# Optimization experiments

Hardware: AMD Instinct MI355X
Metric: run time of the kernel (lower is better)

Reference implementation:

```python
import jax, jax.numpy as jnp
import numpy as np

TAU = 2.0
SG_ALPHA = 4.0  # spikingjelly surrogate.Sigmoid default alpha
BN_EPS = 1e-5


def _spike_fwd(x):
    s = (x >= 0.0).astype(x.dtype)
    return s, x


def _spike_bwd(x, g):
    sg = jax.nn.sigmoid(SG_ALPHA * x)
    return (g * SG_ALPHA * sg * (1.0 - sg),)


@jax.custom_vjp
def spike(x):
    return (x >= 0.0).astype(x.dtype)

spike.defvjp(_spike_fwd, _spike_bwd)


def lif(x_seq, v_th=1.0):
    """MultiStepLIFNode: v += (x - v)/tau (v_reset=0), hard reset, detach_reset.
    x_seq: [T, ...] -> spike train [T, ...]."""
    def step(v, x):
        v = v + (x - v) / TAU
        s = spike(v - v_th)
        v = v * (1.0 - jax.lax.stop_gradient(s))
        return v, s
    v0 = jnp.zeros_like(x_seq[0])
    _, s_seq = jax.lax.scan(step, v0, x_seq)
    return s_seq


def bn1d(x, p):
    """Eval-mode BatchNorm1d over channel dim. x: [M, C, N], p: [4, C] = gamma,beta,mean,var."""
    g, b, m, v = p[0], p[1], p[2], p[3]
    scale = g * jax.lax.rsqrt(v + BN_EPS)
    return (x - m[:, None]) * scale[:, None] + b[:, None]


def setup_inputs() -> dict:
    key = jax.random.key(0)
    ks = jax.random.split(key, 16)
    T, B, C, H, W = 4, 8, 256, 32, 32
    hid = 1024
    wscale = 1.0 / np.sqrt(C)
    inp = {
        "x": jax.random.normal(ks[0], (T, B, C, H, W), jnp.float32),
        "q_w": jax.random.normal(ks[1], (C, C), jnp.float32) * wscale,
        "q_bn": jax.random.uniform(ks[2], (4, C), jnp.float32, 0.1, 1.0),
        "k_w": jax.random.normal(ks[3], (C, C), jnp.float32) * wscale,
        "k_bn": jax.random.uniform(ks[4], (4, C), jnp.float32, 0.1, 1.0),
        "v_w": jax.random.normal(ks[5], (C, C), jnp.float32) * wscale,
        "v_bn": jax.random.uniform(ks[6], (4, C), jnp.float32, 0.1, 1.0),
        "proj_w": jax.random.normal(ks[7], (C, C), jnp.float32) * wscale,
        "proj_b": jax.random.normal(ks[8], (C,), jnp.float32) * 0.01,
        "proj_bn": jax.random.uniform(ks[9], (4, C), jnp.float32, 0.1, 1.0),
        "mlp1_w": jax.random.normal(ks[10], (hid, C), jnp.float32) * wscale,
        "mlp1_b": jax.random.normal(ks[11], (hid,), jnp.float32) * 0.01,
        "mlp1_bn": jax.random.uniform(ks[12], (4, hid), jnp.float32, 0.1, 1.0),
        "mlp2_w": jax.random.normal(ks[13], (C, hid), jnp.float32) * (1.0 / np.sqrt(hid)),
        "mlp2_b": jax.random.normal(ks[14], (C,), jnp.float32) * 0.01,
        "mlp2_bn": jax.random.uniform(ks[15], (4, C), jnp.float32, 0.1, 1.0),
    }
    return inp


def reference(x, q_w, q_bn, k_w, k_bn, v_w, v_bn, proj_w, proj_b, proj_bn,
              mlp1_w, mlp1_b, mlp1_bn, mlp2_w, mlp2_b, mlp2_bn):
    T, B, C, H, W = x.shape
    N = H * W
    heads = 8
    d = C // heads
    scale = 0.125

    # ---- SSA (FB_LiDiff_Attention) ----
    x2 = x.reshape(T * B, C, N)  # conv1x1 input

    def qkv_path(w, p):
        y = jnp.einsum('oc,mcn->mon', w, x2)           # conv1x1, no bias
        y = bn1d(y, p).reshape(T, B, C, N)
        s = lif(y)                                      # [T,B,C,N] spikes
        # -> [T,B,heads,N,d]
        return s.transpose(0, 1, 3, 2).reshape(T, B, N, heads, d).transpose(0, 1, 3, 2, 4)

    q = qkv_path(q_w, q_bn)
    k = qkv_path(k_w, k_bn)
    v = qkv_path(v_w, v_bn)

    kv = jnp.einsum('tbhnd,tbhne->tbhde', k, v)         # k^T @ v  [T,B,h,d,d]
    a = jnp.einsum('tbhnd,tbhde->tbhne', q, kv) * scale  # q @ kv  [T,B,h,N,d]
    a = a.transpose(0, 1, 2, 4, 3).reshape(T, B, C, N)   # transpose(3,4).reshape
    a = lif(a, v_th=0.5)

    p = jnp.einsum('oc,mcn->mon', proj_w, a.reshape(T * B, C, N)) + proj_b[:, None]
    p = bn1d(p, proj_bn).reshape(T, B, C, N)
    ssa = lif(p).reshape(T, B, C, W, H)  # note W,H swap as in source (H==W)

    x = x + ssa

    # ---- MLP (conv1x1 + BN + LIF, x2) ----
    h1 = jnp.einsum('oc,mcn->mon', mlp1_w, x.reshape(T * B, C, N)) + mlp1_b[:, None]
    hid = mlp1_w.shape[0]
    h1 = lif(bn1d(h1, mlp1_bn).reshape(T, B, hid, N))
    h2 = jnp.einsum('oc,mcn->mon', mlp2_w, h1.reshape(T * B, hid, N)) + mlp2_b[:, None]
    h2 = lif(bn1d(h2, mlp2_bn).reshape(T, B, C, N)).reshape(T, B, C, H, W)

    return x + h2
```

## Files before the change

kernel.cpp:

```cpp
#include <hip/hip_runtime.h>
#include <cstdint>
#include <cstddef>

#define TT 4
#define BB 8
#define CC 256
#define NN 1024
#define HEADS 8
#define DD 32
#define FIXCAP 262144u

typedef __attribute__((ext_vector_type(4))) float f32x4;
typedef __attribute__((ext_vector_type(8))) short s16x8;
typedef unsigned short u16;
typedef unsigned int   u32;

__device__ __forceinline__ u16 bf16_rne(float x) {
    u32 u = __float_as_uint(x);
    return (u16)((u + 0x7FFFu + ((u >> 16) & 1u)) >> 16);
}
__device__ __forceinline__ float bf16f(u16 h) {
    return __uint_as_float(((u32)h) << 16);
}

__global__ __launch_bounds__(64) void zero_counters(u32* c) {
    if (threadIdx.x < 4) c[threadIdx.x] = 0;
}


template<int OO, int CIN>
__global__ __launch_bounds__(256) void prep_split_fm(
    const float* __restrict__ src, u16* __restrict__ h, u16* __restrict__ l)
{
    const int id = blockIdx.x * 256 + threadIdx.x;
    if (id >= OO * CIN / 8) return;
    const int o = id / (CIN / 8), kq = id % (CIN / 8);
    const float* p = src + (size_t)o * CIN + kq * 8;
    s16x8 hh, ll;
#pragma unroll
    for (int e = 0; e < 8; ++e) {
        float f = p[e];
        u16 hb = bf16_rne(f);
        hh[e] = (short)hb;
        ll[e] = (short)bf16_rne(f - bf16f(hb));
    }
    const int lane = (kq & 3) * 16 + (o & 15);
    const size_t dst = (((size_t)(o >> 4) * (CIN / 32) + (kq >> 2)) * 64 + lane) * 8;
    *(s16x8*)&h[dst] = hh;
    *(s16x8*)&l[dst] = ll;
}

template<int K, int N>
__global__ __launch_bounds__(256) void trans_split_fm(
    const float* __restrict__ src, u16* __restrict__ dh, u16* __restrict__ dl)
{
    __shared__ float tile[64][65];
    const int tid = threadIdx.x;
    const int n0 = blockIdx.x * 64, k0 = blockIdx.y * 64, m = blockIdx.z;
    for (int i = tid; i < 4096; i += 256) {
        int kk = i >> 6, nn = i & 63;
        tile[kk][nn] = src[((size_t)m * K + k0 + kk) * N + n0 + nn];
    }
    __syncthreads();
    const size_t plane = (size_t)m * (N / 16) * (K / 32) * 512;
    for (int it = tid; it < 512; it += 256) {
        const int nn = it >> 3, kq = it & 7;
        s16x8 hh, ll;
#pragma unroll
        for (int e = 0; e < 8; ++e) {
            float f = tile[kq * 8 + e][nn];
            u16 hb = bf16_rne(f);
            hh[e] = (short)hb;
            ll[e] = (short)bf16_rne(f - bf16f(hb));
        }
        const int n = n0 + nn;
        const int ks = (k0 >> 5) + (kq >> 2), lk = kq & 3;
        const size_t dst = plane + (((size_t)(n >> 4) * (K / 32) + ks) * 64
                                    + lk * 16 + (n & 15)) * 8;
        *(s16x8*)&dh[dst] = hh;
        *(s16x8*)&dl[dst] = ll;
    }
}

template<int K, int N>
__global__ __launch_bounds__(256) void trans_u16_fm(
    const u16* __restrict__ src, u16* __restrict__ dst)
{
    __shared__ u16 tile[64][72];
    const int tid = threadIdx.x;
    const int n0 = blockIdx.x * 64, k0 = blockIdx.y * 64, m = blockIdx.z;
    for (int i = tid; i < 4096; i += 256) {
        int kk = i >> 6, nn = i & 63;
        tile[kk][nn] = src[((size_t)m * K + k0 + kk) * N + n0 + nn];
    }
    __syncthreads();
    const size_t plane = (size_t)m * (N / 16) * (K / 32) * 512;
    for (int it = tid; it < 512; it += 256) {
        const int nn = it >> 3, kq = it & 7;
        s16x8 hh;
#pragma unroll
        for (int e = 0; e < 8; ++e) hh[e] = (short)tile[kq * 8 + e][nn];
        const int n = n0 + nn;
        const int ks = (k0 >> 5) + (kq >> 2), lk = kq & 3;
        const size_t d = plane + (((size_t)(n >> 4) * (K / 32) + ks) * 64
                                  + lk * 16 + (n & 15)) * 8;
        *(s16x8*)&dst[d] = hh;
    }
}

__global__ __launch_bounds__(256) void prep_bn(
    const float* qbn, const float* kbn, const float* vbn, const float* pbn,
    const float* m1bn, const float* m2bn,
    const float* pb, const float* m1b, const float* m2b,
    float2* __restrict__ bnf, double* __restrict__ bnd)
{
    int c = blockIdx.x * 256 + threadIdx.x;
    if (c >= 2304) return;
    const float* bn; int ch, O; double bi = 0.0;
    if (c < 1024) {
        int s = c >> 8; ch = c & 255; O = 256;
        bn = s == 0 ? qbn : s == 1 ? kbn : s == 2 ? vbn : pbn;
        if (s == 3) bi = (double)pb[ch];
    } else if (c < 2048) { ch = c - 1024; O = 1024; bn = m1bn; bi = (double)m1b[ch]; }
    else                 { ch = c - 2048; O = 256;  bn = m2bn; bi = (double)m2b[ch]; }
    double g = (double)bn[0*O+ch], be = (double)bn[1*O+ch];
    double mu = (double)bn[2*O+ch], var = (double)bn[3*O+ch];
    double sd = g / sqrt(var + 1e-5);
    bnf[c] = make_float2((float)sd, (float)((bi - mu) * sd + be));
    bnd[c] = sd;
}

template<bool SPLIT_IN, int CIN, int OUT_MODE, bool TRIPLE, int O>
__global__ __launch_bounds__(256, 2) void conv_kernel(
    const u16* __restrict__ XTH, const u16* __restrict__ XTL,
    const u16* __restrict__ WH0, const u16* __restrict__ WL0,
    const u16* __restrict__ WH1, const u16* __restrict__ WL1,
    const u16* __restrict__ WH2, const u16* __restrict__ WL2,
    const float2* __restrict__ bnf,
    void* __restrict__ O0_, void* __restrict__ O1_, void* __restrict__ O2_,
    const float* __restrict__ base,
    u32* __restrict__ cnt, u32* __restrict__ list)
{
    constexpr float EPS = 3e-4f;
    constexpr u32 OT = TRIPLE ? 12 : O / 64;
    constexpr u32 NWG = OT * 16 * 8;
    constexpr int NS = CIN / 32;
    constexpr u32 KS = (u32)(CIN / 32);
    __shared__ float pre[2 * 64 * 64];

    const int tid  = threadIdx.x;
    const int lane = tid & 63;
    const int wave = tid >> 6;
    const int lr   = lane & 15;
    const int lk   = lane >> 4;

    const u32 orig = blockIdx.x + OT * (blockIdx.y + 16u * blockIdx.z);
    const u32 flat = (orig & 7u) * (NWG >> 3) + (orig >> 3);
    const u32 otile = flat % OT;
    const u32 rem   = flat / OT;
    const int n0 = (int)(rem & 15u) * 64;
    const int b  = (int)(rem >> 4);

    int o0, sel;
    const u16 *WH, *WL;
    void* Out_;
    if constexpr (TRIPLE) {
        sel = (int)(otile >> 2);
        o0 = (int)(otile & 3) * 64;
        WH = sel==0?WH0:sel==1?WH1:WH2;  WL = sel==0?WL0:sel==1?WL1:WL2;
        Out_ = sel==0?O0_:sel==1?O1_:O2_;
    } else {
        sel = 0; o0 = (int)otile * 64; WH = WH0; WL = WL0; Out_ = O0_;
    }
    const int cofs = sel * 256;

    f32x4 acc[4][4];
#pragma unroll
    for (int mf = 0; mf < 4; ++mf)
#pragma unroll
        for (int nf = 0; nf < 4; ++nf)
            acc[mf][nf] = (f32x4){0.f, 0.f, 0.f, 0.f};

    u32 afm[4], bfm[4];
#pragma unroll
    for (int mf = 0; mf < 4; ++mf)
        afm[mf] = ((u32)(o0 / 16 + mf) * KS) * 512u + (u32)lane * 8u;
    const u32 xplane = (u32)(wave * BB + b) * (u32)(NN / 16) * KS * 512u;
#pragma unroll
    for (int nf = 0; nf < 4; ++nf)
        bfm[nf] = xplane + ((u32)(n0 / 16 + nf) * KS) * 512u + (u32)lane * 8u;

    struct Frag { s16x8 aH[4], aL[4], bH[4], bL[4]; };
    Frag f0, f1;

    auto loadstep = [&](int ks, Frag& f) {
        const u32 ko = (u32)ks * 512u;
#pragma unroll
        for (int mf = 0; mf < 4; ++mf) {
            f.aH[mf] = *(const s16x8*)&WH[(size_t)(afm[mf] + ko)];
            f.aL[mf] = *(const s16x8*)&WL[(size_t)(afm[mf] + ko)];
        }
#pragma unroll
        for (int nf = 0; nf < 4; ++nf) {
            f.bH[nf] = *(const s16x8*)&XTH[(size_t)(bfm[nf] + ko)];
            if constexpr (SPLIT_IN)
                f.bL[nf] = *(const s16x8*)&XTL[(size_t)(bfm[nf] + ko)];
        }
    };
    auto compute = [&](Frag& f) {
        __builtin_amdgcn_s_setprio(1);
#pragma unroll
        for (int mf = 0; mf < 4; ++mf)
#pragma unroll
            for (int nf = 0; nf < 4; ++nf) {
                acc[mf][nf] = __builtin_amdgcn_mfma_f32_16x16x32_bf16(
                    f.aH[mf], f.bH[nf], acc[mf][nf], 0, 0, 0);
                acc[mf][nf] = __builtin_amdgcn_mfma_f32_16x16x32_bf16(
                    f.aL[mf], f.bH[nf], acc[mf][nf], 0, 0, 0);
                if constexpr (SPLIT_IN)
                    acc[mf][nf] = __builtin_amdgcn_mfma_f32_16x16x32_bf16(
                        f.aH[mf], f.bL[nf], acc[mf][nf], 0, 0, 0);
            }
        __builtin_amdgcn_s_setprio(0);
    };

    loadstep(0, f0);
#pragma unroll
    for (int ks = 0; ks < NS; ++ks) {
        if ((ks & 1) == 0) {
            if (ks + 1 < NS) loadstep(ks + 1, f1);
            compute(f0);
        } else {
            if (ks + 1 < NS) loadstep(ks + 1, f0);
            compute(f1);
        }
    }

    const int nl = tid & 63;
    const int og = wave;

    auto dump = [&](int slot) {
#pragma unroll
        for (int mf = 0; mf < 4; ++mf)
#pragma unroll
            for (int nf = 0; nf < 4; ++nf)
#pragma unroll
                for (int r = 0; r < 4; ++r)
                    pre[(size_t)(slot * 64 + mf * 16 + lk * 4 + r) * 64
                        + nf * 16 + lr] = acc[mf][nf][r];
    };

    float2 sc[16];
#pragma unroll
    for (int i = 0; i < 16; ++i) sc[i] = bnf[cofs + o0 + og * 16 + i];

    unsigned flags = 0;
    float vst[16];
    u32 spA = 0, spB = 0;

    auto do_round = [&](int tbase) {
#pragma unroll
        for (int i = 0; i < 16; ++i) {
            const int o = o0 + og * 16 + i;
            float v = (tbase == 0) ? 0.f : vst[i];
#pragma unroll
            for (int dt = 0; dt < 2; ++dt) {
                const int t = tbase + dt;
                float val = fmaf(pre[(size_t)(dt * 64 + og * 16 + i) * 64 + nl], sc[i].x, sc[i].y);
                v = v + (val - v) * 0.5f;
                if (fabsf(v - 1.0f) < EPS) flags |= (1u << i);
                float s = (v >= 1.0f) ? 1.f : 0.f;
                if constexpr (OUT_MODE == 2) {
                    const u32 bit = (s > 0.5f) ? 1u : 0u;
                    if (tbase == 0) spA |= bit << (dt * 16 + i);
                    else            spB |= bit << (dt * 16 + i);
                } else {
                    const size_t idx = (((size_t)t * BB + b) * O + o) * NN + n0 + nl;
                    if constexpr (OUT_MODE == 0)
                        ((u16*)Out_)[idx] = (s > 0.5f) ? (u16)0x3F80 : (u16)0;
                    else
                        ((float*)Out_)[idx] = base[idx] + s;
                }
                v *= (1.f - s);
            }
            vst[i] = v;
        }
    };

    __syncthreads();
    if (wave < 2) dump(wave);
    __syncthreads();
    do_round(0);
    __syncthreads();
    if (wave >= 2) dump(wave - 2);
    __syncthreads();
    do_round(2);

    if constexpr (OUT_MODE == 2) {
        __syncthreads();
        u16* lds16 = (u16*)pre;
#pragma unroll
        for (int dt = 0; dt < 2; ++dt)
#pragma unroll
            for (int i = 0; i < 16; ++i) {
                const int ol = og * 16 + i;
                const int loc = ((nl >> 4) * 2 + (ol >> 5)) * 512
                              + ((ol >> 3) & 3) * 128 + (nl & 15) * 8 + (ol & 7);
                lds16[dt * 4096 + loc] =
                    ((spA >> (dt * 16 + i)) & 1u) ? (u16)0x3F80 : (u16)0;
                lds16[(2 + dt) * 4096 + loc] =
                    ((spB >> (dt * 16 + i)) & 1u) ? (u16)0x3F80 : (u16)0;
            }
        __syncthreads();
        constexpr u32 KO = (u32)(O / 32);
        for (int idx2 = tid; idx2 < 2048; idx2 += 256) {
            const int t = idx2 >> 9, rem2 = idx2 & 511;
            const int c = rem2 >> 6, pos = (rem2 & 63) * 8;
            const int nt = c >> 1, ob = c & 1;
            const size_t gb = (((size_t)(t * BB + b) * (NN / 16) + (n0 / 16 + nt)) * KO
                               + (o0 / 32 + ob)) * 512 + pos;
            *(s16x8*)&((u16*)Out_)[gb] = *(const s16x8*)&lds16[t * 4096 + c * 512 + pos];
        }
    }

    if (flags) {
#pragma unroll 1
        for (int i = 0; i < 16; ++i) {
            if (!(flags & (1u << i))) continue;
            const int o = o0 + og * 16 + i;
            const u32 ent = ((u32)sel << 23) | ((u32)b << 20) | ((u32)o << 10)
                          | (u32)(n0 + nl);
            const u32 idx = atomicAdd(cnt, 1u);
            if (idx < FIXCAP) list[idx] = ent;
        }
    }
}

template<bool XE_BF16, bool XE_FM, int CIN, int OUT_MODE, int O>
__global__ __launch_bounds__(64) void fixup_kernel(
    const u32* __restrict__ cnt, const u32* __restrict__ list,
    const void* __restrict__ Xe_,
    const float* __restrict__ Wx0, const float* __restrict__ Wx1,
    const float* __restrict__ Wx2,
    const float* __restrict__ bnr0, const float* __restrict__ bnr1,
    const float* __restrict__ bnr2, const float* __restrict__ bias,
    const double* __restrict__ bnd,
    void* __restrict__ O0_, void* __restrict__ O1_, void* __restrict__ O2_,
    const float* __restrict__ base)
{
    const u32 c0 = *cnt;
    const u32 count = c0 > FIXCAP ? FIXCAP : c0;
    const int lane = threadIdx.x;
    for (u32 e = blockIdx.x; e < count; e += gridDim.x) {
        const u32 ent = list[e];
        const int n = (int)(ent & 1023u);
        const int o = (int)((ent >> 10) & 1023u);
        const int b = (int)((ent >> 20) & 7u);
        const int sel = (int)(ent >> 23);
        const float* Wx  = sel == 0 ? Wx0  : (sel == 1 ? Wx1  : Wx2);
        const float* bnr = sel == 0 ? bnr0 : (sel == 1 ? bnr1 : bnr2);
        void* Out_ = sel == 0 ? O0_ : (sel == 1 ? O1_ : O2_);
        double p[4] = {0.0, 0.0, 0.0, 0.0};
        for (int k = lane; k < CIN; k += 64) {
            const double w = (double)Wx[(size_t)o * CIN + k];
#pragma unroll
            for (int t = 0; t < 4; ++t) {
                size_t xi;
                if constexpr (XE_FM)
                    xi = (((size_t)(t * BB + b) * (NN / 16) + (n >> 4)) * (CIN / 32)
                          + (k >> 5)) * 512 + ((k >> 3) & 3) * 128 + (n & 15) * 8 + (k & 7);
                else
                    xi = ((size_t)(t * BB + b) * CIN + k) * NN + n;
                double xv;
                if constexpr (XE_BF16) xv = (double)bf16f(((const u16*)Xe_)[xi]);
                else                   xv = (double)((const float*)Xe_)[xi];
                p[t] += w * xv;
            }
        }
#pragma unroll
        for (int off = 32; off; off >>= 1)
#pragma unroll
            for (int t = 0; t < 4; ++t) p[t] += __shfl_down(p[t], off);
        if (lane == 0) {
            const double scale = bnd[(OUT_MODE == 0 ? sel * 256 : 0) + o];
            const double be = (double)bnr[1 * O + o];
            const double mu = (double)bnr[2 * O + o];
            double bi = 0.0;
            if constexpr (OUT_MODE != 0) bi = (double)bias[o];
            double v = 0.0;
#pragma unroll
            for (int t = 0; t < TT; ++t) {
                const double val = (p[t] + bi - mu) * scale + be;
                v = v + (val - v) * 0.5;
                const double sd = (v >= 1.0) ? 1.0 : 0.0;
                if constexpr (OUT_MODE == 2) {
                    const size_t fm = (((size_t)(t * BB + b) * (NN / 16) + (n >> 4))
                                       * (O / 32) + (o >> 5)) * 512
                                    + ((o >> 3) & 3) * 128 + (n & 15) * 8 + (o & 7);
                    ((u16*)Out_)[fm] = (sd > 0.5) ? (u16)0x3F80 : (u16)0;
                } else {
                    const size_t idx = (((size_t)t * BB + b) * O + o) * NN + n;
                    if constexpr (OUT_MODE == 0)
                        ((u16*)Out_)[idx] = (sd > 0.5) ? (u16)0x3F80 : (u16)0;
                    else
                        ((float*)Out_)[idx] = (float)((double)base[idx] + sd);
                }
                v = v * (1.0 - sd);
            }
        }
    }
}

__global__ __launch_bounds__(256) void kv_mfma(
    const u16* __restrict__ k_s, const u16* __restrict__ v_s,
    float* __restrict__ kv)
{
    const int lane = threadIdx.x & 63;
    const int wave = threadIdx.x >> 6;
    const int unit = blockIdx.x * 4 + wave;
    const int h = unit & 7;
    const int m = unit >> 3;
    const int lr = lane & 15, lk = lane >> 4;
    const size_t base = ((size_t)m * CC + h * DD) * NN;

    f32x4 acc[2][2];
#pragma unroll
    for (int mt = 0; mt < 2; ++mt)
#pragma unroll
        for (int nt = 0; nt < 2; ++nt)
            acc[mt][nt] = (f32x4){0.f, 0.f, 0.f, 0.f};

#pragma unroll 4
    for (int ks = 0; ks < 32; ++ks) {
        s16x8 a[2], bf[2];
#pragma unroll
        for (int mt = 0; mt < 2; ++mt)
            a[mt] = *(const s16x8*)&k_s[base + (size_t)(mt * 16 + lr) * NN
                                         + ks * 32 + lk * 8];
#pragma unroll
        for (int nt = 0; nt < 2; ++nt)
            bf[nt] = *(const s16x8*)&v_s[base + (size_t)(nt * 16 + lr) * NN
                                          + ks * 32 + lk * 8];
#pragma unroll
        for (int mt = 0; mt < 2; ++mt)
#pragma unroll
            for (int nt = 0; nt < 2; ++nt)
                acc[mt][nt] = __builtin_amdgcn_mfma_f32_16x16x32_bf16(
                    a[mt], bf[nt], acc[mt][nt], 0, 0, 0);
    }
#pragma unroll
    for (int mt = 0; mt < 2; ++mt)
#pragma unroll
        for (int nt = 0; nt < 2; ++nt)
#pragma unroll
            for (int r = 0; r < 4; ++r)
                kv[(size_t)unit * 1024 + (mt * 16 + lk * 4 + r) * 32
                   + nt * 16 + lr] = acc[mt][nt][r];
}

__global__ __launch_bounds__(256) void attn_a_lif(
    const u16* __restrict__ q_s, const float* __restrict__ kv,
    u16* __restrict__ a_s)
{
    __shared__ u16 qt[TT][32][64];
    __shared__ float kvs[TT][32][32];
    const int tid = threadIdx.x;
    const int n0 = blockIdx.x * 64;
    const int h  = blockIdx.y;
    const int b  = blockIdx.z;

    for (int i = tid; i < TT * 32 * 64 / 4; i += 256) {
        const int t = i >> 9, rem = i & 511;
        const int d = rem >> 4, n4 = rem & 15;
        const size_t g = (((size_t)t * BB + b) * CC + h * DD + d) * NN + n0 + n4 * 4;
        *(ushort4*)&qt[t][d][n4 * 4] = *(const ushort4*)&q_s[g];
    }
    for (int i = tid; i < TT * 32 * 32 / 4; i += 256) {
        const int t = i >> 8, rem = i & 255;
        const int d = rem >> 3, e4 = rem & 7;
        const size_t g = (((size_t)t * BB + b) * HEADS + h) * 1024 + d * 32 + e4 * 4;
        *(float4*)&kvs[t][d][e4 * 4] = *(const float4*)&kv[g];
    }
    __syncthreads();

    const int nl = tid & 63;
    const int eg = tid >> 6;
#pragma unroll
    for (int ei = 0; ei < 8; ++ei) {
        const int e = eg * 8 + ei;
        float val[TT];
#pragma unroll
        for (int t = 0; t < TT; ++t) {
            float s = 0.f;
#pragma unroll 8
            for (int d = 0; d < 32; ++d)
                s += bf16f(qt[t][d][nl]) * kvs[t][d][e];
            val[t] = s * 0.125f;
        }
        float v = 0.f;
#pragma unroll
        for (int t = 0; t < TT; ++t) {
            v = v + (val[t] - v) * 0.5f;
            float s = (v >= 0.5f) ? 1.f : 0.f;
            a_s[(((size_t)t * BB + b) * CC + h * DD + e) * NN + n0 + nl] =
                (s > 0.5f) ? (u16)0x3F80 : (u16)0;
            v = v * (1.f - s);
        }
    }
}

extern "C" void kernel_launch(void* const* d_in, const int* in_sizes, int n_in,
                              void* d_out, int out_size, void* d_ws, size_t ws_size,
                              hipStream_t stream)
{
    const float* x       = (const float*)d_in[0];
    const float* q_w     = (const float*)d_in[1];
    const float* q_bn    = (const float*)d_in[2];
    const float* k_w     = (const float*)d_in[3];
    const float* k_bn    = (const float*)d_in[4];
    const float* v_w     = (const float*)d_in[5];
    const float* v_bn    = (const float*)d_in[6];
    const float* proj_w  = (const float*)d_in[7];
    const float* proj_b  = (const float*)d_in[8];
    const float* proj_bn = (const float*)d_in[9];
    const float* mlp1_w  = (const float*)d_in[10];
    const float* mlp1_b  = (const float*)d_in[11];
    const float* mlp1_bn = (const float*)d_in[12];
    const float* mlp2_w  = (const float*)d_in[13];
    const float* mlp2_b  = (const float*)d_in[14];
    const float* mlp2_bn = (const float*)d_in[15];

    const size_t SZ = (size_t)TT * BB * CC * NN;
    const size_t U = SZ * 2;
    char* ws = (char*)d_ws;
    u16*   xTh  = (u16*)(ws);
    u16*   xTl  = (u16*)(ws + U);
    u16*   q_s  = (u16*)(ws + 2*U);
    u16*   k_s  = (u16*)(ws + 3*U);
    u16*   v_s  = (u16*)(ws + 4*U);
    u16*   a_s  = (u16*)(ws);
    u16*   aT   = (u16*)(ws + U);
    float* x_new= (float*)(ws + 2*U);
    u16*   xnTh = (u16*)(ws + 4*U);
    u16*   xnTl = (u16*)(ws + 5*U);
    u16*   h1T  = (u16*)(ws + 10*U);
    char* wp = ws + 14*U;
    float* kvb = (float*)wp; wp += (size_t)262144 * 4;
    u16* qh  = (u16*)wp; wp += 65536 * 2;  u16* ql  = (u16*)wp; wp += 65536 * 2;
    u16* kh  = (u16*)wp; wp += 65536 * 2;  u16* kl  = (u16*)wp; wp += 65536 * 2;
    u16* vh  = (u16*)wp; wp += 65536 * 2;  u16* vl  = (u16*)wp; wp += 65536 * 2;
    u16* ph  = (u16*)wp; wp += 65536 * 2;  u16* pl  = (u16*)wp; wp += 65536 * 2;
    u16* m1h = (u16*)wp; wp += 262144 * 2; u16* m1l = (u16*)wp; wp += 262144 * 2;
    u16* m2h = (u16*)wp; wp += 262144 * 2; u16* m2l = (u16*)wp; wp += 262144 * 2;
    float2* bnf = (float2*)wp; wp += 2304 * 8;
    double* bnd = (double*)wp; wp += 2304 * 8;
    u32* cnts = (u32*)wp; wp += 4 * 4;
    u32* list0 = (u32*)wp; wp += FIXCAP * 4;
    u32* list1 = (u32*)wp; wp += FIXCAP * 4;
    u32* list2 = (u32*)wp; wp += FIXCAP * 4;
    u32* list3 = (u32*)wp;

    dim3 blk(256);

    zero_counters<<<dim3(1), dim3(64), 0, stream>>>(cnts);

    prep_split_fm<256, 256>  <<<dim3(32),  blk, 0, stream>>>(q_w,    qh,  ql);
    prep_split_fm<256, 256>  <<<dim3(32),  blk, 0, stream>>>(k_w,    kh,  kl);
    prep_split_fm<256, 256>  <<<dim3(32),  blk, 0, stream>>>(v_w,    vh,  vl);
    prep_split_fm<256, 256>  <<<dim3(32),  blk, 0, stream>>>(proj_w, ph,  pl);
    prep_split_fm<1024, 256> <<<dim3(128), blk, 0, stream>>>(mlp1_w, m1h, m1l);
    prep_split_fm<256, 1024> <<<dim3(128), blk, 0, stream>>>(mlp2_w, m2h, m2l);
    trans_split_fm<256, 1024><<<dim3(16, 4, 32), blk, 0, stream>>>(x, xTh, xTl);
    prep_bn<<<dim3(9), blk, 0, stream>>>(q_bn, k_bn, v_bn, proj_bn, mlp1_bn,
                                         mlp2_bn, proj_b, mlp1_b, mlp2_b, bnf, bnd);

    conv_kernel<true, 256, 0, true, 256><<<dim3(12, 16, 8), blk, 0, stream>>>(
        xTh, xTl, qh, ql, kh, kl, vh, vl, bnf, q_s, k_s, v_s, nullptr,
        cnts + 0, list0);
    fixup_kernel<false, false, 256, 0, 256><<<dim3(1024), dim3(64), 0, stream>>>(
        cnts + 0, list0, x, q_w, k_w, v_w, q_bn, k_bn, v_bn, nullptr, bnd,
        q_s, k_s, v_s, nullptr);

    kv_mfma<<<dim3(64), blk, 0, stream>>>(k_s, v_s, kvb);
    attn_a_lif<<<dim3(16, 8, 8), blk, 0, stream>>>(q_s, kvb, a_s);
    trans_u16_fm<256, 1024><<<dim3(16, 4, 32), blk, 0, stream>>>(a_s, aT);

    conv_kernel<false, 256, 1, false, 256><<<dim3(4, 16, 8), blk, 0, stream>>>(
        aT, nullptr, ph, pl, nullptr, nullptr, nullptr, nullptr,
        bnf + 768, x_new, nullptr, nullptr, x, cnts + 1, list1);
    fixup_kernel<true, false, 256, 1, 256><<<dim3(1024), dim3(64), 0, stream>>>(
        cnts + 1, list1, a_s, proj_w, nullptr, nullptr, proj_bn, nullptr,
        nullptr, proj_b, bnd + 768, x_new, nullptr, nullptr, x);

    trans_split_fm<256, 1024><<<dim3(16, 4, 32), blk, 0, stream>>>(x_new, xnTh, xnTl);

    conv_kernel<true, 256, 2, false, 1024><<<dim3(16, 16, 8), blk, 0, stream>>>(
        xnTh, xnTl, m1h, m1l, nullptr, nullptr, nullptr, nullptr,
        bnf + 1024, h1T, nullptr, nullptr, nullptr, cnts + 2, list2);
    fixup_kernel<false, false, 256, 2, 1024><<<dim3(1024), dim3(64), 0, stream>>>(
        cnts + 2, list2, x_new, mlp1_w, nullptr, nullptr, mlp1_bn, nullptr,
        nullptr, mlp1_b, bnd + 1024, h1T, nullptr, nullptr, nullptr);

    conv_kernel<false, 1024, 3, false, 256><<<dim3(4, 16, 8), blk, 0, stream>>>(
        h1T, nullptr, m2h, m2l, nullptr, nullptr, nullptr, nullptr,
        bnf + 2048, d_out, nullptr, nullptr, x_new, cnts + 3, list3);
    fixup_kernel<true, true, 1024, 3, 256><<<dim3(1024), dim3(64), 0, stream>>>(
        cnts + 3, list3, h1T, mlp2_w, nullptr, nullptr, mlp2_bn, nullptr,
        nullptr, mlp2_b, bnd + 2048, d_out, nullptr, nullptr, x_new);
}
```

Before: 376.9 us.

## Fuse fragment-major transposes into attention and proj conv epilogues

Removes the standalone trans_u16_fm and trans_split_fm launches. attn_a_lif now stages its spikes in shared memory and writes the fragment-major aT layout directly. The proj conv (and its fixup) now emits the hi/lo bf16 split of x_new in fragment-major form via a new LDS staging buffer. This saves two kernel launches and their extra global read/write passes, at the cost of more LDS use in the proj conv (an extra 32KB), which may lower occupancy.

```diff
diff --git a/kernel.cpp b/kernel.cpp
--- a/kernel.cpp
+++ b/kernel.cpp
@@ -79,32 +79,6 @@
                                     + lk * 16 + (n & 15)) * 8;
         *(s16x8*)&dh[dst] = hh;
         *(s16x8*)&dl[dst] = ll;
-    }
-}
-
-template<int K, int N>
-__global__ __launch_bounds__(256) void trans_u16_fm(
-    const u16* __restrict__ src, u16* __restrict__ dst)
-{
-    __shared__ u16 tile[64][72];
-    const int tid = threadIdx.x;
-    const int n0 = blockIdx.x * 64, k0 = blockIdx.y * 64, m = blockIdx.z;
-    for (int i = tid; i < 4096; i += 256) {
-        int kk = i >> 6, nn = i & 63;
-        tile[kk][nn] = src[((size_t)m * K + k0 + kk) * N + n0 + nn];
-    }
-    __syncthreads();
-    const size_t plane = (size_t)m * (N / 16) * (K / 32) * 512;
-    for (int it = tid; it < 512; it += 256) {
-        const int nn = it >> 3, kq = it & 7;
-        s16x8 hh;
-#pragma unroll
-        for (int e = 0; e < 8; ++e) hh[e] = (short)tile[kq * 8 + e][nn];
-        const int n = n0 + nn;
-        const int ks = (k0 >> 5) + (kq >> 2), lk = kq & 3;
-        const size_t d = plane + (((size_t)(n >> 4) * (K / 32) + ks) * 64
-                                  + lk * 16 + (n & 15)) * 8;
-        *(s16x8*)&dst[d] = hh;
     }
 }
 
@@ -138,6 +112,7 @@
     const u16* __restrict__ WH2, const u16* __restrict__ WL2,
     const float2* __restrict__ bnf,
     void* __restrict__ O0_, void* __restrict__ O1_, void* __restrict__ O2_,
+    u16* __restrict__ OutH, u16* __restrict__ OutL,
     const float* __restrict__ base,
     u32* __restrict__ cnt, u32* __restrict__ list)
 {
@@ -147,6 +122,7 @@
     constexpr int NS = CIN / 32;
     constexpr u32 KS = (u32)(CIN / 32);
     __shared__ float pre[2 * 64 * 64];
+    __shared__ u16 xnst[OUT_MODE == 1 ? 16384 : 4];
 
     const int tid  = threadIdx.x;
     const int lane = tid & 63;
@@ -280,10 +256,33 @@
                         ((u16*)Out_)[idx] = (s > 0.5f) ? (u16)0x3F80 : (u16)0;
                     else
                         ((float*)Out_)[idx] = base[idx] + s;
+                    if constexpr (OUT_MODE == 1) {
+                        const float xn = ((float*)Out_)[idx];
+                        const u16 hb = bf16_rne(xn);
+                        const int och = (og * 16 + i) >> 5;
+                        const int loc = ((dt * 4 + (nl >> 4)) * 2 + och) * 512
+                                      + ((o >> 3) & 3) * 128 + (nl & 15) * 8 + (o & 7);
+                        xnst[loc] = hb;
+                        xnst[8192 + loc] = bf16_rne(xn - bf16f(hb));
+                    }
                 }
                 v *= (1.f - s);
             }
             vst[i] = v;
+        }
+    };
+
+    auto fmwrite = [&](int tbase) {
+        for (int idx2 = tid; idx2 < 2048; idx2 += 256) {
+            const int p = idx2 >> 10, r1 = idx2 & 1023;
+            const int dt = r1 >> 9, r2 = r1 & 511;
+            const int ntile = r2 >> 7, och = (r2 >> 6) & 1, pos = (r2 & 63) * 8;
+            const int t = tbase + dt;
+            const size_t gb = (((size_t)(t * BB + b) * (NN / 16) + (n0 / 16 + ntile))
+                               * (CC / 32) + (o0 / 32 + och)) * 512 + pos;
+            u16* dst = p ? OutL : OutH;
+            *(s16x8*)&dst[gb] =
+                *(const s16x8*)&xnst[p * 8192 + ((dt * 4 + ntile) * 2 + och) * 512 + pos];
         }
     };
 
@@ -293,8 +292,14 @@
     do_round(0);
     __syncthreads();
     if (wave >= 2) dump(wave - 2);
+    if constexpr (OUT_MODE == 1) fmwrite(0);
     __syncthreads();
     do_round(2);
+
+    if constexpr (OUT_MODE == 1) {
+        __syncthreads();
+        fmwrite(2);
+    }
 
     if constexpr (OUT_MODE == 2) {
         __syncthreads();
@@ -346,6 +351,7 @@
     const float* __restrict__ bnr2, const float* __restrict__ bias,
     const double* __restrict__ bnd,
     void* __restrict__ O0_, void* __restrict__ O1_, void* __restrict__ O2_,
+    u16* __restrict__ OutH, u16* __restrict__ OutL,
     const float* __restrict__ base)
 {
     const u32 c0 = *cnt;
@@ -404,6 +410,15 @@
                         ((u16*)Out_)[idx] = (sd > 0.5) ? (u16)0x3F80 : (u16)0;
                     else
                         ((float*)Out_)[idx] = (float)((double)base[idx] + sd);
+                    if constexpr (OUT_MODE == 1) {
+                        const float xn = ((float*)Out_)[idx];
+                        const u16 hb = bf16_rne(xn);
+                        const size_t fm = (((size_t)(t * BB + b) * (NN / 16) + (n >> 4))
+                                           * (CC / 32) + (o >> 5)) * 512
+                                        + ((o >> 3) & 3) * 128 + (n & 15) * 8 + (o & 7);
+                        OutH[fm] = hb;
+                        OutL[fm] = bf16_rne(xn - bf16f(hb));
+                    }
                 }
                 v = v * (1.0 - sd);
             }
@@ -460,10 +475,11 @@
 
 __global__ __launch_bounds__(256) void attn_a_lif(
     const u16* __restrict__ q_s, const float* __restrict__ kv,
-    u16* __restrict__ a_s)
+    u16* __restrict__ a_s, u16* __restrict__ aT)
 {
     __shared__ u16 qt[TT][32][64];
     __shared__ float kvs[TT][32][32];
+    __shared__ u16 ast[TT][4][512];
     const int tid = threadIdx.x;
     const int n0 = blockIdx.x * 64;
     const int h  = blockIdx.y;
@@ -502,10 +518,19 @@
         for (int t = 0; t < TT; ++t) {
             v = v + (val[t] - v) * 0.5f;
             float s = (v >= 0.5f) ? 1.f : 0.f;
-            a_s[(((size_t)t * BB + b) * CC + h * DD + e) * NN + n0 + nl] =
-                (s > 0.5f) ? (u16)0x3F80 : (u16)0;
+            const u16 sp = (s > 0.5f) ? (u16)0x3F80 : (u16)0;
+            a_s[(((size_t)t * BB + b) * CC + h * DD + e) * NN + n0 + nl] = sp;
+            ast[t][nl >> 4][((e >> 3) & 3) * 128 + (nl & 15) * 8 + (e & 7)] = sp;
             v = v * (1.f - s);
         }
+    }
+    __syncthreads();
+    for (int i = tid; i < 1024; i += 256) {
+        const int t = i >> 8, r2 = i & 255;
+        const int ntile = r2 >> 6, pos = (r2 & 63) * 8;
+        const size_t gb = (((size_t)(t * BB + b) * (NN / 16) + (n0 / 16 + ntile))
+                           * (CC / 32) + h) * 512 + pos;
+        *(s16x8*)&aT[gb] = *(const s16x8*)&ast[t][ntile][pos];
     }
 }
 
@@ -575,36 +600,37 @@
                                          mlp2_bn, proj_b, mlp1_b, mlp2_b, bnf, bnd);
 
     conv_kernel<true, 256, 0, true, 256><<<dim3(12, 16, 8), blk, 0, stream>>>(
-        xTh, xTl, qh, ql, kh, kl, vh, vl, bnf, q_s, k_s, v_s, nullptr,
-        cnts + 0, list0);
+        xTh, xTl, qh, ql, kh, kl, vh, vl, bnf, q_s, k_s, v_s,
+        nullptr, nullptr, nullptr, cnts + 0, list0);
     fixup_kernel<false, false, 256, 0, 256><<<dim3(1024), dim3(64), 0, stream>>>(
         cnts + 0, list0, x, q_w, k_w, v_w, q_bn, k_bn, v_bn, nullptr, bnd,
-        q_s, k_s, v_s, nullptr);
+        q_s, k_s, v_s, nullptr, nullptr, nullptr);
 
     kv_mfma<<<dim3(64), blk, 0, stream>>>(k_s, v_s, kvb);
-    attn_a_lif<<<dim3(16, 8, 8), blk, 0, stream>>>(q_s, kvb, a_s);
-    trans_u16_fm<256, 1024><<<dim3(16, 4, 32), blk, 0, stream>>>(a_s, aT);
+    attn_a_lif<<<dim3(16, 8, 8), blk, 0, stream>>>(q_s, kvb, a_s, aT);
 
     conv_kernel<false, 256, 1, false, 256><<<dim3(4, 16, 8), blk, 0, stream>>>(
         aT, nullptr, ph, pl, nullptr, nullptr, nullptr, nullptr,
-        bnf + 768, x_new, nullptr, nullptr, x, cnts + 1, list1);
+        bnf + 768, x_new, nullptr, nullptr, xnTh, xnTl, x, cnts + 1, list1);
     fixup_kernel<true, false, 256, 1, 256><<<dim3(1024), dim3(64), 0, stream>>>(
         cnts + 1, list1, a_s, proj_w, nullptr, nullptr, proj_bn, nullptr,
-        nullptr, proj_b, bnd + 768, x_new, nullptr, nullptr, x);
-
-    trans_split_fm<256, 1024><<<dim3(16, 4, 32), blk, 0, stream>>>(x_new, xnTh, xnTl);
+        nullptr, proj_b, bnd + 768, x_new, nullptr, nullptr, xnTh, xnTl, x);
 
     conv_kernel<true, 256, 2, false, 1024><<<dim3(16, 16, 8), blk, 0, stream>>>(
         xnTh, xnTl, m1h, m1l, nullptr, nullptr, nullptr, nullptr,
-        bnf + 1024, h1T, nullptr, nullptr, nullptr, cnts + 2, list2);
+        bnf + 1024, h1T, nullptr, nullptr, nullptr, nullptr, nullptr,
+        cnts + 2, list2);
     fixup_kernel<false, false, 256, 2, 1024><<<dim3(1024), dim3(64), 0, stream>>>(
         cnts + 2, list2, x_new, mlp1_w, nullptr, nullptr, mlp1_bn, nullptr,
-        nullptr, mlp1_b, bnd + 1024, h1T, nullptr, nullptr, nullptr);
+        nullptr, mlp1_b, bnd + 1024, h1T, nullptr, nullptr, nullptr, nullptr,
+        nullptr);
 
     conv_kernel<false, 1024, 3, false, 256><<<dim3(4, 16, 8), blk, 0, stream>>>(
         h1T, nullptr, m2h, m2l, nullptr, nullptr, nullptr, nullptr,
-        bnf + 2048, d_out, nullptr, nullptr, x_new, cnts + 3, list3);
+        bnf + 2048, d_out, nullptr, nullptr, nullptr, nullptr, x_new,
+        cnts + 3, list3);
     fixup_kernel<true, true, 1024, 3, 256><<<dim3(1024), dim3(64), 0, stream>>>(
         cnts + 3, list3, h1T, mlp2_w, nullptr, nullptr, mlp2_bn, nullptr,
-        nullptr, mlp2_b, bnd + 2048, d_out, nullptr, nullptr, x_new);
-}
+        nullptr, mlp2_b, bnd + 2048, d_out, nullptr, nullptr, nullptr, nullptr,
+        x_new);
+}
```

Result: faster. 363.8 us (-3.5%).
